# Kernel optimization log

Measured on AMD Instinct MI355X. Metric: run time of the kernel, lower is better.

Reference implementation:

```python
import jax, jax.numpy as jnp
import numpy as np

D = 1024   # dim_model
H = 16     # num_heads
DH = D // H  # per-head dim for k and v
B, S = 2, 2048
EPS = 1e-5


def layer_norm(x, g, b):
    mu = jnp.mean(x, axis=-1, keepdims=True)
    var = jnp.var(x, axis=-1, keepdims=True)
    return (x - mu) * jax.lax.rsqrt(var + EPS) * g + b


def setup_inputs() -> dict:
    key = jax.random.key(0)
    ks = jax.random.split(key, 8)
    s_d = 1.0 / np.sqrt(D)
    inp = {
        "x": jax.random.normal(ks[0], (B, S, D), dtype=jnp.float32),
        # stacked per-head projections, [H, D, DH] (torch Linear weight.T per head)
        "wq": jax.random.uniform(ks[1], (H, D, DH), jnp.float32, -s_d, s_d),
        "wk": jax.random.uniform(ks[2], (H, D, DH), jnp.float32, -s_d, s_d),
        "wv": jax.random.uniform(ks[3], (H, D, DH), jnp.float32, -s_d, s_d),
        "wo": jax.random.uniform(ks[4], (D, D), jnp.float32, -s_d, s_d),
        "w1": jax.random.uniform(ks[5], (D, D), jnp.float32, -s_d, s_d),  # FFN hidden == dim_model per source
        "w2": jax.random.uniform(ks[6], (D, D), jnp.float32, -s_d, s_d),
        "ln1_g": jnp.ones((D,), jnp.float32), "ln1_b": jnp.zeros((D,), jnp.float32),
        "ln2_g": jnp.ones((D,), jnp.float32), "ln2_b": jnp.zeros((D,), jnp.float32),
        "ln3_g": jnp.ones((D,), jnp.float32), "ln3_b": jnp.zeros((D,), jnp.float32),
    }
    return inp


def reference(x, wq, wk, wv, wo, w1, w2, ln1_g, ln1_b, ln2_g, ln2_b, ln3_g, ln3_b):
    residual = x
    h = layer_norm(x, ln1_g, ln1_b)  # pre_attention_norm
    # batched multi-head attention (equivalent to per-head loop + concat)
    q = jnp.einsum("bsd,hdk->bhsk", h, wq)
    k = jnp.einsum("bsd,hdk->bhsk", h, wk)
    v = jnp.einsum("bsd,hdk->bhsk", h, wv)
    scores = jnp.einsum("bhsk,bhtk->bhst", q, k) / jnp.sqrt(jnp.float32(DH))
    attn = jax.nn.softmax(scores, axis=-1)
    ctx = jnp.einsum("bhst,bhtk->bhsk", attn, v)        # [B,H,S,DH]
    concat = ctx.transpose(0, 2, 1, 3).reshape(x.shape[0], x.shape[1], -1)  # head concat order
    h = concat @ wo
    h = h + residual
    h = layer_norm(h, ln2_g, ln2_b)  # post_attention_norm (dropout is identity, rate=0)
    residual = h
    ffn = jnp.maximum(h @ w1, 0.0) @ w2
    h = ffn + residual
    h = layer_norm(h, ln3_g, ln3_b)  # post_ffn_norm
    return h
```

## Files before the change

### kernel.cpp

```cpp
#include <hip/hip_runtime.h>
#include <stdint.h>

typedef unsigned short u16;
typedef __attribute__((ext_vector_type(8))) short short8;
typedef __attribute__((ext_vector_type(4))) short short4v;
typedef __attribute__((ext_vector_type(4))) float f32x4;

#define DEV static __device__ __forceinline__

constexpr int DMODEL = 1024;
constexpr int SEQ = 2048;

DEV u16 f2b(float f){
  uint32_t u = __float_as_uint(f);
  u += 0x7FFF + ((u >> 16) & 1);
  return (u16)(u >> 16);
}

DEV float b2f(u16 b){ uint32_t u = ((uint32_t)b)<<16; return __uint_as_float(u); }

#define AS1(p) ((const __attribute__((address_space(1))) void*)(p))
#define AS3(p) ((__attribute__((address_space(3))) void*)(p))
#define GLOAD_LDS16(g, l) __builtin_amdgcn_global_load_lds(AS1(g), AS3(l), 16, 0, 0)
#define LDSADDR(p) ((uint32_t)(size_t)((__attribute__((address_space(3))) void*)(p)))

DEV short4v ds_tr16(uint32_t a){
  short4v r;
  asm volatile("ds_read_b64_tr_b16 %0, %1" : "=v"(r) : "v"(a) : "memory");
  return r;
}

DEV void pswap(uint32_t &a, uint32_t &b){
  asm("v_permlane32_swap_b32 %0, %1":"+v"(a),"+v"(b));
  asm("v_permlane16_swap_b32 %0, %1":"+v"(a),"+v"(b));
}

DEV uint32_t cvtpk(float lo, float hi){
  uint32_t r; asm("v_cvt_pk_bf16_f32 %0, %1, %2":"=v"(r):"v"(lo),"v"(hi)); return r;
}

__global__ __launch_bounds__(256) void transpose_all(
    const float* __restrict__ wq, const float* __restrict__ wk,
    const float* __restrict__ wv, const float* __restrict__ wo,
    const float* __restrict__ w1, const float* __restrict__ w2,
    u16* __restrict__ WqkvT, u16* __restrict__ WoT,
    u16* __restrict__ W1T, u16* __restrict__ W2T){
  __shared__ float tile[64][65];
  int bid = blockIdx.x;
  int j = threadIdx.x & 63, i0 = threadIdx.x >> 6;
  if(bid < 768){
    int xb = bid & 15, z = bid >> 4;
    int p = z >> 4, h = z & 15;
    const float* src = (p==0?wq:(p==1?wk:wv)) + (size_t)h*1024*64;
    float sc = (p==0) ? 0.18033688011112042f : 1.0f;
    int r0 = xb*64;
    for(int i=i0;i<64;i+=4) tile[i][j] = src[(size_t)(r0+i)*64 + j];
    __syncthreads();
    u16* drow = WqkvT + ((size_t)p*1024 + h*64)*1024;
    for(int jj=i0;jj<64;jj+=4) drow[(size_t)jj*1024 + r0 + j] = f2b(tile[j][jj]*sc);
  } else {
    int t = bid - 768;
    int which = t >> 8; t &= 255;
    const float* src = which==0?wo:(which==1?w1:w2);
    u16* dst = which==0?WoT:(which==1?W1T:W2T);
    int r0 = (t&15)*64, c0 = (t>>4)*64;
    for(int i=i0;i<64;i+=4) tile[i][j] = src[(size_t)(r0+i)*1024 + c0 + j];
    __syncthreads();
    for(int jj=i0;jj<64;jj+=4) dst[(size_t)(c0+jj)*1024 + r0 + j] = f2b(tile[j][jj]);
  }
}

__global__ __launch_bounds__(256) void ln_kernel(
    const float* __restrict__ in, const float* __restrict__ g, const float* __restrict__ bb,
    u16* __restrict__ outb, float* __restrict__ outf){
  int row = blockIdx.x, tid = threadIdx.x;
  const float4* x4 = (const float4*)(in + (size_t)row*DMODEL);
  float4 v = x4[tid];
  float s  = v.x+v.y+v.z+v.w;
  float ss = v.x*v.x + v.y*v.y + v.z*v.z + v.w*v.w;
  #pragma unroll
  for(int m=1;m<64;m<<=1){ s += __shfl_xor(s,m); ss += __shfl_xor(ss,m); }
  __shared__ float red[8];
  int w = tid>>6;
  if((tid&63)==0){ red[w]=s; red[4+w]=ss; }
  __syncthreads();
  s  = red[0]+red[1]+red[2]+red[3];
  ss = red[4]+red[5]+red[6]+red[7];
  float mu  = s*(1.f/DMODEL);
  float var = ss*(1.f/DMODEL) - mu*mu;
  float rs  = rsqrtf(var + 1e-5f);
  float4 gv = ((const float4*)g)[tid];
  float4 bv = ((const float4*)bb)[tid];
  float y0=(v.x-mu)*rs*gv.x+bv.x, y1=(v.y-mu)*rs*gv.y+bv.y;
  float y2=(v.z-mu)*rs*gv.z+bv.z, y3=(v.w-mu)*rs*gv.w+bv.w;
  if(outb){ ushort4 o = make_ushort4(f2b(y0),f2b(y1),f2b(y2),f2b(y3));
            ((ushort4*)outb)[(size_t)row*(DMODEL/4) + tid] = o; }
  if(outf){ ((float4*)outf)[(size_t)row*(DMODEL/4) + tid] = make_float4(y0,y1,y2,y3); }
}

template<int MODE>
__global__ __launch_bounds__(256) void gemm_bt(
    const u16* __restrict__ A, const u16* __restrict__ BT, int M, int N, int K,
    float* __restrict__ outf, u16* __restrict__ outb, const float* __restrict__ resf,
    const u16* __restrict__ resb,
    u16* __restrict__ oq, u16* __restrict__ ok, u16* __restrict__ ov){
  __shared__ u16 lsA[2][4096];
  __shared__ u16 lsB[2][4096];
  int n0 = blockIdx.x*128, m0 = blockIdx.y*128;
  int tid = threadIdx.x, lane = tid&63, w = tid>>6;
  int wr = w>>1, wc = w&1, rq = lane&15, hk = lane>>4;
  int o0 = tid*16, o1 = 4096 + tid*16;
  const u16* aS0 = A  + (size_t)(m0 + (o0>>6))*K + ((o0&63)>>1);
  const u16* aS1 = A  + (size_t)(m0 + (o1>>6))*K + ((o1&63)>>1);
  const u16* bS0 = BT + (size_t)(n0 + (o0>>6))*K + ((o0&63)>>1);
  const u16* bS1 = BT + (size_t)(n0 + (o1>>6))*K + ((o1&63)>>1);
  int nk = K>>5;
  f32x4 acc[4][4] = {};
  GLOAD_LDS16(aS0, &lsA[0][w*512]);
  GLOAD_LDS16(aS1, &lsA[0][2048 + w*512]);
  GLOAD_LDS16(bS0, &lsB[0][w*512]);
  GLOAD_LDS16(bS1, &lsB[0][2048 + w*512]);
  #pragma unroll 2
  for(int kt=0; kt<nk; ++kt){
    __syncthreads();
    if(kt+1 < nk){
      int nb = (kt+1)&1;
      GLOAD_LDS16(aS0 + (kt+1)*32, &lsA[nb][w*512]);
      GLOAD_LDS16(aS1 + (kt+1)*32, &lsA[nb][2048 + w*512]);
      GLOAD_LDS16(bS0 + (kt+1)*32, &lsB[nb][w*512]);
      GLOAD_LDS16(bS1 + (kt+1)*32, &lsB[nb][2048 + w*512]);
    }
    const u16* la = &lsA[kt&1][0];
    const u16* lb = &lsB[kt&1][0];
    short8 aF[4], bF[4];
    #pragma unroll
    for(int m=0;m<4;++m) aF[m] = *(const short8*)(la + (wr*64 + m*16 + rq)*32 + hk*8);
    #pragma unroll
    for(int n=0;n<4;++n) bF[n] = *(const short8*)(lb + (wc*64 + n*16 + rq)*32 + hk*8);
    __builtin_amdgcn_s_setprio(1);
    #pragma unroll
    for(int m=0;m<4;++m){
      #pragma unroll
      for(int n=0;n<4;++n)
        acc[m][n] = __builtin_amdgcn_mfma_f32_16x16x32_bf16(aF[m], bF[n], acc[m][n], 0,0,0);
    }
    __builtin_amdgcn_s_setprio(0);
  }
  #pragma unroll
  for(int m=0;m<4;++m){
    #pragma unroll
    for(int n=0;n<4;++n){
      int rb = m0 + wr*64 + m*16 + (hk<<2);
      int c  = n0 + wc*64 + n*16 + rq;
      #pragma unroll
      for(int qq=0;qq<4;++qq){
        int r = rb+qq; float val = acc[m][n][qq];
        if constexpr(MODE==1){
          int proj=c>>10, n1=c&1023, h=n1>>6, d2=n1&63;
          int b=r>>11, si=r&2047;
          u16* dst = proj==0?oq:(proj==1?ok:ov);
          dst[(((size_t)(b*16+h))*SEQ + si)*64 + d2] = f2b(val);
        } else if constexpr(MODE==2){
          outf[(size_t)r*N + c] = val + resf[(size_t)r*N + c];
        } else if constexpr(MODE==3){
          outb[(size_t)r*N + c] = f2b(val>0.f?val:0.f);
        } else if constexpr(MODE==4){
          outf[(size_t)r*N + c] = val + b2f(resb[(size_t)r*N + c]);
        } else {
          outb[(size_t)r*N + c] = f2b(val);
        }
      }
    }
  }
}

__global__ __launch_bounds__(256) void attn_kernel(
    const u16* __restrict__ q, const u16* __restrict__ k, const u16* __restrict__ v,
    u16* __restrict__ concat){
  __shared__ u16 lsK[2][4096];
  __shared__ u16 lsV[2][4096];
  int qt = blockIdx.x, bh = blockIdx.y;
  const u16* qp = q + (size_t)bh*SEQ*64;
  const u16* kp = k + (size_t)bh*SEQ*64;
  const u16* vp = v + (size_t)bh*SEQ*64;
  int tid=threadIdx.x, lane=tid&63, w=tid>>6;
  int rq = lane&15, hk = lane>>4;
  const uint32_t sw = (uint32_t)((rq&7)<<4);

  short8 aQ[2];
  {
    const u16* qrow = qp + (size_t)(qt*64 + w*16 + rq)*64 + hk*8;
    aQ[0] = *(const short8*)(qrow);
    aQ[1] = *(const short8*)(qrow + 32);
  }
  short8 bOnes;
  #pragma unroll
  for(int j=0;j<8;++j) bOnes[j] = (short)0x3F80;

  int o0 = tid*16,        kr0 = o0>>7;
  int o1 = 4096 + tid*16, kr1 = o1>>7;
  int koff0 = kr0*64 + ((((o0&127) ^ ((kr0&7)<<4)))>>1);
  int koff1 = kr1*64 + ((((o1&127) ^ ((kr1&7)<<4)))>>1);
  auto vdec = [](int c)->int{
    int t  = ((c>>5)<<2) | ((c&7)>>1);
    int d8 = (((c>>3)&3)<<1) | (c&1);
    return t*64 + d8*8;
  };
  int voff0 = vdec(tid), voff1 = vdec(256+tid);

  f32x4 accO[4] = {};
  f32x4 accL = {};

  GLOAD_LDS16(kp + koff0, &lsK[0][0   + w*512]);
  GLOAD_LDS16(kp + koff1, &lsK[0][2048+ w*512]);
  GLOAD_LDS16(vp + voff0, &lsV[0][0   + w*512]);
  GLOAD_LDS16(vp + voff1, &lsV[0][2048+ w*512]);

  int cur = 0;
  for(int kt=0; kt<SEQ/64; ++kt){
    __syncthreads();
    if(kt+1 < SEQ/64){
      int b = cur^1;
      const u16* ksrc = kp + (kt+1)*4096;
      const u16* vsrc = vp + (kt+1)*4096;
      GLOAD_LDS16(ksrc + koff0, &lsK[b][0   + w*512]);
      GLOAD_LDS16(ksrc + koff1, &lsK[b][2048+ w*512]);
      GLOAD_LDS16(vsrc + voff0, &lsV[b][0   + w*512]);
      GLOAD_LDS16(vsrc + voff1, &lsV[b][2048+ w*512]);
    }
    const char* kb = (const char*)&lsK[cur][0];
    short8 bK[4][2];
    #pragma unroll
    for(int ts=0;ts<4;++ts){
      uint32_t rb = (uint32_t)((ts*16+rq)*128);
      bK[ts][0] = *(const short8*)(kb + rb + (((uint32_t)(hk<<4)) ^ sw));
      bK[ts][1] = *(const short8*)(kb + rb + ((64u|(uint32_t)(hk<<4)) ^ sw));
    }
    f32x4 z[4];
    __builtin_amdgcn_s_setprio(1);
    #pragma unroll
    for(int ts=0;ts<4;++ts){
      f32x4 zz = {};
      zz = __builtin_amdgcn_mfma_f32_16x16x32_bf16(bK[ts][0], aQ[0], zz, 0,0,0);
      zz = __builtin_amdgcn_mfma_f32_16x16x32_bf16(bK[ts][1], aQ[1], zz, 0,0,0);
      z[ts] = zz;
    }
    __builtin_amdgcn_s_setprio(0);
    uint32_t vA = LDSADDR(&lsV[cur][0]) + (uint32_t)(hk*1024 + rq*2);
    short4v vL[2][4][2];
    #pragma unroll
    for(int kh=0;kh<2;++kh){
      #pragma unroll
      for(int ds=0;ds<4;++ds){
        vL[kh][ds][0] = ds_tr16(vA + kh*4096 + ds*128);
        vL[kh][ds][1] = ds_tr16(vA + kh*4096 + ds*128 + 512);
      }
    }
    #pragma unroll
    for(int ts=0;ts<4;++ts){
      #pragma unroll
      for(int r=0;r<4;++r)
        z[ts][r] = __builtin_exp2f(z[ts][r]);
    }
    uint32_t u00=cvtpk(z[0][0],z[0][1]), u01=cvtpk(z[0][2],z[0][3]);
    uint32_t u10=cvtpk(z[1][0],z[1][1]), u11=cvtpk(z[1][2],z[1][3]);
    uint32_t u20=cvtpk(z[2][0],z[2][1]), u21=cvtpk(z[2][2],z[2][3]);
    uint32_t u30=cvtpk(z[3][0],z[3][1]), u31=cvtpk(z[3][2],z[3][3]);
    pswap(u00,u10); pswap(u01,u11);
    pswap(u20,u30); pswap(u21,u31);
    union U8 { uint32_t d[4]; short8 v; } ap0, ap1;
    ap0.d[0]=u00; ap0.d[1]=u01; ap0.d[2]=u10; ap0.d[3]=u11;
    ap1.d[0]=u20; ap1.d[1]=u21; ap1.d[2]=u30; ap1.d[3]=u31;
    asm volatile("s_waitcnt lgkmcnt(0)" ::: "memory");
    __builtin_amdgcn_sched_barrier(0);
    __builtin_amdgcn_s_setprio(1);
    #pragma unroll
    for(int kh=0;kh<2;++kh){
      short8 aP = kh ? ap1.v : ap0.v;
      accL = __builtin_amdgcn_mfma_f32_16x16x32_bf16(aP, bOnes, accL, 0,0,0);
      #pragma unroll
      for(int ds=0;ds<4;++ds){
        short8 bV = __builtin_shufflevector(vL[kh][ds][0], vL[kh][ds][1], 0,1,2,3,4,5,6,7);
        accO[ds] = __builtin_amdgcn_mfma_f32_16x16x32_bf16(aP, bV, accO[ds], 0,0,0);
      }
    }
    __builtin_amdgcn_s_setprio(0);
    cur ^= 1;
  }
  int b = bh>>4, h = bh&15;
  #pragma unroll
  for(int r=0;r<4;++r){
    float inv = 1.f / accL[r];
    int si = qt*64 + w*16 + hk*4 + r;
    #pragma unroll
    for(int ds=0;ds<4;++ds){
      int c = h*64 + ds*16 + rq;
      concat[((size_t)b*SEQ + si)*DMODEL + c] = f2b(accO[ds][r] * inv);
    }
  }
}

extern "C" void kernel_launch(void* const* d_in, const int* in_sizes, int n_in,
                              void* d_out, int out_size, void* d_ws, size_t ws_size,
                              hipStream_t stream){
  (void)in_sizes; (void)n_in; (void)out_size; (void)ws_size;
  const float* x    = (const float*)d_in[0];
  const float* wq   = (const float*)d_in[1];
  const float* wk   = (const float*)d_in[2];
  const float* wv   = (const float*)d_in[3];
  const float* wo   = (const float*)d_in[4];
  const float* w1   = (const float*)d_in[5];
  const float* w2   = (const float*)d_in[6];
  const float* ln1g = (const float*)d_in[7];
  const float* ln1b = (const float*)d_in[8];
  const float* ln2g = (const float*)d_in[9];
  const float* ln2b = (const float*)d_in[10];
  const float* ln3g = (const float*)d_in[11];
  const float* ln3b = (const float*)d_in[12];
  float* out = (float*)d_out;

  char* ws = (char*)d_ws; size_t off = 0;
  auto alloc = [&](size_t b)->char*{ char* p = ws + off; off += (b + 255) & ~(size_t)255; return p; };
  u16*   WqkvT = (u16*)  alloc((size_t)3072*1024*2);
  u16*   WoT   = (u16*)  alloc((size_t)1024*1024*2);
  u16*   W1T   = (u16*)  alloc((size_t)1024*1024*2);
  u16*   W2T   = (u16*)  alloc((size_t)1024*1024*2);
  u16*   h1    = (u16*)  alloc((size_t)4096*1024*2);
  u16*   qb    = (u16*)  alloc((size_t)4194304*2);
  u16*   kb    = (u16*)  alloc((size_t)4194304*2);
  u16*   vb    = (u16*)  alloc((size_t)4194304*2);
  u16*   cc    = (u16*)  alloc((size_t)4096*1024*2);
  float* r1    = (float*)alloc((size_t)4096*1024*4);
  u16*   h2b   = (u16*)  alloc((size_t)4096*1024*2);
  float* r2    = (float*)alloc((size_t)4096*1024*4);
  u16*   ffn1  = h1;

  transpose_all<<<1536,256,0,stream>>>(wq,wk,wv,wo,w1,w2, WqkvT,WoT,W1T,W2T);

  ln_kernel<<<4096,256,0,stream>>>(x, ln1g, ln1b, h1, nullptr);
  gemm_bt<1><<<dim3(24,32),256,0,stream>>>(h1,WqkvT,4096,3072,1024,
      nullptr,nullptr,nullptr,nullptr, qb,kb,vb);
  attn_kernel<<<dim3(32,32),256,0,stream>>>(qb,kb,vb,cc);
  gemm_bt<2><<<dim3(8,32),256,0,stream>>>(cc,WoT,4096,1024,1024,
      r1,nullptr,x,nullptr, nullptr,nullptr,nullptr);
  ln_kernel<<<4096,256,0,stream>>>(r1, ln2g, ln2b, h2b, nullptr);
  gemm_bt<3><<<dim3(8,32),256,0,stream>>>(h2b,W1T,4096,1024,1024,
      nullptr,ffn1,nullptr,nullptr, nullptr,nullptr,nullptr);
  gemm_bt<4><<<dim3(8,32),256,0,stream>>>(ffn1,W2T,4096,1024,1024,
      r2,nullptr,nullptr,h2b, nullptr,nullptr,nullptr);
  ln_kernel<<<4096,256,0,stream>>>(r2, ln3g, ln3b, nullptr, out);
}
```

Measured before the change: 206.1 us.

## Halve attention KV tile to raise occupancy; simplify QKV scatter epilogue

The attention kernel now processes 32 keys per iteration instead of 64. This halves LDS buffers and per-iteration registers, and a launch bound of 8 blocks per CU is added to raise occupancy. Separately, the QKV projection epilogue computes one base pointer per thread and stores with constant offsets, replacing per-element index decoding. The smaller tile doubles loop iterations and barriers, and it shortens the prefetch distance per sync.

```diff
diff --git a/kernel.cpp b/kernel.cpp
--- a/kernel.cpp
+++ b/kernel.cpp
@@ -146,39 +146,52 @@
     }
     __builtin_amdgcn_s_setprio(0);
   }
-  #pragma unroll
-  for(int m=0;m<4;++m){
-    #pragma unroll
-    for(int n=0;n<4;++n){
-      int rb = m0 + wr*64 + m*16 + (hk<<2);
-      int c  = n0 + wc*64 + n*16 + rq;
+  if constexpr(MODE==1){
+    int proj = n0 >> 10;
+    u16* dsel = proj==0?oq:(proj==1?ok:ov);
+    int h0 = ((n0 & 1023) >> 6) + wc;
+    int bb = m0 >> 11;
+    int si0 = (m0 & 2047) + wr*64 + hk*4;
+    u16* obase = dsel + (((size_t)(bb*16 + h0))*SEQ + si0)*64 + rq;
+    #pragma unroll
+    for(int m=0;m<4;++m){
       #pragma unroll
-      for(int qq=0;qq<4;++qq){
-        int r = rb+qq; float val = acc[m][n][qq];
-        if constexpr(MODE==1){
-          int proj=c>>10, n1=c&1023, h=n1>>6, d2=n1&63;
-          int b=r>>11, si=r&2047;
-          u16* dst = proj==0?oq:(proj==1?ok:ov);
-          dst[(((size_t)(b*16+h))*SEQ + si)*64 + d2] = f2b(val);
-        } else if constexpr(MODE==2){
-          outf[(size_t)r*N + c] = val + resf[(size_t)r*N + c];
-        } else if constexpr(MODE==3){
-          outb[(size_t)r*N + c] = f2b(val>0.f?val:0.f);
-        } else if constexpr(MODE==4){
-          outf[(size_t)r*N + c] = val + b2f(resb[(size_t)r*N + c]);
-        } else {
-          outb[(size_t)r*N + c] = f2b(val);
+      for(int n=0;n<4;++n){
+        #pragma unroll
+        for(int qq=0;qq<4;++qq)
+          obase[(size_t)(m*16+qq)*64 + n*16] = f2b(acc[m][n][qq]);
+      }
+    }
+  } else {
+    #pragma unroll
+    for(int m=0;m<4;++m){
+      #pragma unroll
+      for(int n=0;n<4;++n){
+        int rb = m0 + wr*64 + m*16 + (hk<<2);
+        int c  = n0 + wc*64 + n*16 + rq;
+        #pragma unroll
+        for(int qq=0;qq<4;++qq){
+          int r = rb+qq; float val = acc[m][n][qq];
+          if constexpr(MODE==2){
+            outf[(size_t)r*N + c] = val + resf[(size_t)r*N + c];
+          } else if constexpr(MODE==3){
+            outb[(size_t)r*N + c] = f2b(val>0.f?val:0.f);
+          } else if constexpr(MODE==4){
+            outf[(size_t)r*N + c] = val + b2f(resb[(size_t)r*N + c]);
+          } else {
+            outb[(size_t)r*N + c] = f2b(val);
+          }
         }
       }
     }
   }
 }
 
-__global__ __launch_bounds__(256) void attn_kernel(
+__global__ __launch_bounds__(256, 8) void attn_kernel(
     const u16* __restrict__ q, const u16* __restrict__ k, const u16* __restrict__ v,
     u16* __restrict__ concat){
-  __shared__ u16 lsK[2][4096];
-  __shared__ u16 lsV[2][4096];
+  __shared__ u16 lsK[2][2048];
+  __shared__ u16 lsV[2][2048];
   int qt = blockIdx.x, bh = blockIdx.y;
   const u16* qp = q + (size_t)bh*SEQ*64;
   const u16* kp = k + (size_t)bh*SEQ*64;
@@ -197,49 +210,38 @@
   #pragma unroll
   for(int j=0;j<8;++j) bOnes[j] = (short)0x3F80;
 
-  int o0 = tid*16,        kr0 = o0>>7;
-  int o1 = 4096 + tid*16, kr1 = o1>>7;
-  int koff0 = kr0*64 + ((((o0&127) ^ ((kr0&7)<<4)))>>1);
-  int koff1 = kr1*64 + ((((o1&127) ^ ((kr1&7)<<4)))>>1);
-  auto vdec = [](int c)->int{
-    int t  = ((c>>5)<<2) | ((c&7)>>1);
-    int d8 = (((c>>3)&3)<<1) | (c&1);
-    return t*64 + d8*8;
-  };
-  int voff0 = vdec(tid), voff1 = vdec(256+tid);
+  int o = tid*16, kr = o>>7;
+  const u16* kS = kp + kr*64 + ((((o&127) ^ ((kr&7)<<4)))>>1);
+  int vt  = ((tid>>5)<<2) | ((tid&7)>>1);
+  int vd8 = (((tid>>3)&3)<<1) | (tid&1);
+  const u16* vS = vp + vt*64 + vd8*8;
 
   f32x4 accO[4] = {};
   f32x4 accL = {};
 
-  GLOAD_LDS16(kp + koff0, &lsK[0][0   + w*512]);
-  GLOAD_LDS16(kp + koff1, &lsK[0][2048+ w*512]);
-  GLOAD_LDS16(vp + voff0, &lsV[0][0   + w*512]);
-  GLOAD_LDS16(vp + voff1, &lsV[0][2048+ w*512]);
+  GLOAD_LDS16(kS, &lsK[0][w*512]);
+  GLOAD_LDS16(vS, &lsV[0][w*512]);
 
   int cur = 0;
-  for(int kt=0; kt<SEQ/64; ++kt){
+  for(int kt=0; kt<SEQ/32; ++kt){
     __syncthreads();
-    if(kt+1 < SEQ/64){
-      int b = cur^1;
-      const u16* ksrc = kp + (kt+1)*4096;
-      const u16* vsrc = vp + (kt+1)*4096;
-      GLOAD_LDS16(ksrc + koff0, &lsK[b][0   + w*512]);
-      GLOAD_LDS16(ksrc + koff1, &lsK[b][2048+ w*512]);
-      GLOAD_LDS16(vsrc + voff0, &lsV[b][0   + w*512]);
-      GLOAD_LDS16(vsrc + voff1, &lsV[b][2048+ w*512]);
+    if(kt+1 < SEQ/32){
+      int nb = cur^1;
+      GLOAD_LDS16(kS + (kt+1)*2048, &lsK[nb][w*512]);
+      GLOAD_LDS16(vS + (kt+1)*2048, &lsV[nb][w*512]);
     }
     const char* kb = (const char*)&lsK[cur][0];
-    short8 bK[4][2];
-    #pragma unroll
-    for(int ts=0;ts<4;++ts){
+    short8 bK[2][2];
+    #pragma unroll
+    for(int ts=0;ts<2;++ts){
       uint32_t rb = (uint32_t)((ts*16+rq)*128);
       bK[ts][0] = *(const short8*)(kb + rb + (((uint32_t)(hk<<4)) ^ sw));
       bK[ts][1] = *(const short8*)(kb + rb + ((64u|(uint32_t)(hk<<4)) ^ sw));
     }
-    f32x4 z[4];
+    f32x4 z[2];
     __builtin_amdgcn_s_setprio(1);
     #pragma unroll
-    for(int ts=0;ts<4;++ts){
+    for(int ts=0;ts<2;++ts){
       f32x4 zz = {};
       zz = __builtin_amdgcn_mfma_f32_16x16x32_bf16(bK[ts][0], aQ[0], zz, 0,0,0);
       zz = __builtin_amdgcn_mfma_f32_16x16x32_bf16(bK[ts][1], aQ[1], zz, 0,0,0);
@@ -247,42 +249,31 @@
     }
     __builtin_amdgcn_s_setprio(0);
     uint32_t vA = LDSADDR(&lsV[cur][0]) + (uint32_t)(hk*1024 + rq*2);
-    short4v vL[2][4][2];
-    #pragma unroll
-    for(int kh=0;kh<2;++kh){
-      #pragma unroll
-      for(int ds=0;ds<4;++ds){
-        vL[kh][ds][0] = ds_tr16(vA + kh*4096 + ds*128);
-        vL[kh][ds][1] = ds_tr16(vA + kh*4096 + ds*128 + 512);
-      }
-    }
-    #pragma unroll
-    for(int ts=0;ts<4;++ts){
+    short4v vL[4][2];
+    #pragma unroll
+    for(int ds=0;ds<4;++ds){
+      vL[ds][0] = ds_tr16(vA + ds*128);
+      vL[ds][1] = ds_tr16(vA + ds*128 + 512);
+    }
+    #pragma unroll
+    for(int ts=0;ts<2;++ts){
       #pragma unroll
       for(int r=0;r<4;++r)
         z[ts][r] = __builtin_exp2f(z[ts][r]);
     }
     uint32_t u00=cvtpk(z[0][0],z[0][1]), u01=cvtpk(z[0][2],z[0][3]);
     uint32_t u10=cvtpk(z[1][0],z[1][1]), u11=cvtpk(z[1][2],z[1][3]);
-    uint32_t u20=cvtpk(z[2][0],z[2][1]), u21=cvtpk(z[2][2],z[2][3]);
-    uint32_t u30=cvtpk(z[3][0],z[3][1]), u31=cvtpk(z[3][2],z[3][3]);
     pswap(u00,u10); pswap(u01,u11);
-    pswap(u20,u30); pswap(u21,u31);
-    union U8 { uint32_t d[4]; short8 v; } ap0, ap1;
-    ap0.d[0]=u00; ap0.d[1]=u01; ap0.d[2]=u10; ap0.d[3]=u11;
-    ap1.d[0]=u20; ap1.d[1]=u21; ap1.d[2]=u30; ap1.d[3]=u31;
+    union U8 { uint32_t d[4]; short8 v; } ap;
+    ap.d[0]=u00; ap.d[1]=u01; ap.d[2]=u10; ap.d[3]=u11;
     asm volatile("s_waitcnt lgkmcnt(0)" ::: "memory");
     __builtin_amdgcn_sched_barrier(0);
     __builtin_amdgcn_s_setprio(1);
-    #pragma unroll
-    for(int kh=0;kh<2;++kh){
-      short8 aP = kh ? ap1.v : ap0.v;
-      accL = __builtin_amdgcn_mfma_f32_16x16x32_bf16(aP, bOnes, accL, 0,0,0);
-      #pragma unroll
-      for(int ds=0;ds<4;++ds){
-        short8 bV = __builtin_shufflevector(vL[kh][ds][0], vL[kh][ds][1], 0,1,2,3,4,5,6,7);
-        accO[ds] = __builtin_amdgcn_mfma_f32_16x16x32_bf16(aP, bV, accO[ds], 0,0,0);
-      }
+    accL = __builtin_amdgcn_mfma_f32_16x16x32_bf16(ap.v, bOnes, accL, 0,0,0);
+    #pragma unroll
+    for(int ds=0;ds<4;++ds){
+      short8 bV = __builtin_shufflevector(vL[ds][0], vL[ds][1], 0,1,2,3,4,5,6,7);
+      accO[ds] = __builtin_amdgcn_mfma_f32_16x16x32_bf16(ap.v, bV, accO[ds], 0,0,0);
     }
     __builtin_amdgcn_s_setprio(0);
     cur ^= 1;
```

Result: slower. 233.5 us (+13.3%).
